# Optimization experiments

Measured on AMD Instinct MI355X. Metric: run time of the kernel, lower is better.

## Reference

```python
import jax, jax.numpy as jnp
import numpy as np

NAMES = ['tempo', 'chord', 'barbeat', 'type', 'pitch', 'duration', 'velocity']
VOCABS = [56, 135, 18, 4, 87, 18, 25]
EMBS = [128, 256, 64, 32, 512, 128, 128]
B, S, D, H, L, FF = 2, 2048, 512, 8, 8, 2048
HD = D // H
EPS = 1e-6


def _layernorm(x, g, b):
    m = x.mean(-1, keepdims=True)
    v = ((x - m) ** 2).mean(-1, keepdims=True)
    return (x - m) / jnp.sqrt(v + 1e-5) * g + b


def _rope(x, cos, sin):
    x1, x2 = jnp.split(x, 2, -1)
    return x * cos + jnp.concatenate([-x2, x1], -1) * sin


def _causal_linear_attn(q, k, v):
    # kernelized causal linear attention: phi = elu + 1, cumulative-sum normalization
    q = jax.nn.elu(q) + 1.0
    k = jax.nn.elu(k) + 1.0
    kv = jnp.cumsum(jnp.einsum('bshd,bshm->bshdm', k, v), axis=1)  # [B,S,H,HD,HD]
    z = 1.0 / (jnp.einsum('bshd,bshd->bsh', q, jnp.cumsum(k, axis=1)) + EPS)
    return jnp.einsum('bshd,bshdm->bshm', q, kv) * z[..., None]


def _forward(inputs, target, emb_tables, in_W, in_b, Wq, bq, Wk, bk, Wv, bv, Wo, bo,
             ln1_g, ln1_b, ln2_g, ln2_b, W1, b1, W2, b2, norm_g, norm_b, pWs, pbs, catW, catb):
    # multi-field embedding, each scaled by sqrt(d_emb) (CPEmbedding)
    embs = [emb_tables[i][inputs[..., i]] * jnp.sqrt(jnp.float32(EMBS[i])) for i in range(7)]
    x = jnp.concatenate(embs, -1) @ in_W + in_b  # [B,S,D]
    # PositionalEncoding: original indexes pe at position seq_len -> single d_model vector
    div = jnp.exp(jnp.arange(0, D, 2, dtype=jnp.float32) * (-np.log(10000.0) / D))
    pe = jnp.zeros((D,), jnp.float32).at[0::2].set(jnp.sin(S * div)).at[1::2].set(jnp.cos(S * div))
    x = x + pe
    # rotary tables for head_dim
    inv_freq = 1.0 / (10000.0 ** (jnp.arange(0, HD, 2, dtype=jnp.float32) / HD))
    fr = jnp.arange(S, dtype=jnp.float32)[:, None] * inv_freq[None, :]
    ang = jnp.concatenate([fr, fr], -1)  # [S,HD]
    cos = jnp.cos(ang)[None, :, None, :]
    sin = jnp.sin(ang)[None, :, None, :]
    for l in range(L):
        q = (x @ Wq[l] + bq[l]).reshape(B, S, H, HD)
        k = (x @ Wk[l] + bk[l]).reshape(B, S, H, HD)
        v = (x @ Wv[l] + bv[l]).reshape(B, S, H, HD)
        q = _rope(q, cos, sin)
        k = _rope(k, cos, sin)
        a = _causal_linear_attn(q, k, v).reshape(B, S, D) @ Wo[l] + bo[l]
        x = x + a
        y = x = _layernorm(x, ln1_g[l], ln1_b[l])
        y = jax.nn.gelu(y @ W1[l] + b1[l], approximate=False) @ W2[l] + b2[l]
        x = _layernorm(x + y, ln2_g[l], ln2_b[l])
    x = _layernorm(x, norm_g, norm_b)
    # MultiProj with teacher-forced type embedding (target branch)
    emb_t = emb_tables[3][target[..., 3]] * jnp.sqrt(jnp.float32(EMBS[3]))
    proj_type = (x @ pWs[3] + pbs[3]) * jnp.sqrt(jnp.float32(VOCABS[3]))  # from pre-concat x
    xc = jnp.concatenate([x, emb_t], -1) @ catW + catb
    outs = []
    for i in range(7):
        if i == 3:
            outs.append(proj_type)
        else:
            outs.append((xc @ pWs[i] + pbs[i]) * jnp.sqrt(jnp.float32(VOCABS[i])))
    return jnp.concatenate(outs, -1)  # [B,S,sum(VOCABS)=343]


def setup_inputs():
    key = jax.random.key(0)
    kit = iter(jax.random.split(key, 64))
    s = 0.02
    d = {}
    d['inputs'] = jax.random.randint(next(kit), (B, S, 7), 0, 4)
    d['target'] = jax.random.randint(next(kit), (B, S, 7), 0, 4)
    for i, n in enumerate(NAMES):
        d['emb_' + n] = jax.random.normal(next(kit), (VOCABS[i], EMBS[i]), jnp.float32) * s
    E = sum(EMBS)
    d['in_W'] = jax.random.normal(next(kit), (E, D)) * s
    d['in_b'] = jnp.zeros((D,))
    for nm, sh in [('Wq', (L, D, D)), ('Wk', (L, D, D)), ('Wv', (L, D, D)), ('Wo', (L, D, D)), ('W1', (L, D, FF)), ('W2', (L, FF, D))]:
        d[nm] = jax.random.normal(next(kit), sh) * s
    for nm, sh in [('bq', (L, D)), ('bk', (L, D)), ('bv', (L, D)), ('bo', (L, D)), ('b1', (L, FF)), ('b2', (L, D)), ('ln1_b', (L, D)), ('ln2_b', (L, D)), ('norm_b', (D,)), ('catb', (D,))]:
        d[nm] = jnp.zeros(sh)
    d['ln1_g'] = jnp.ones((L, D))
    d['ln2_g'] = jnp.ones((L, D))
    d['norm_g'] = jnp.ones((D,))
    for i, n in enumerate(NAMES):
        d['pW_' + n] = jax.random.normal(next(kit), (D, VOCABS[i])) * s
        d['pb_' + n] = jnp.zeros((VOCABS[i],))
    d['catW'] = jax.random.normal(next(kit), (D + 32, D)) * s
    return d


def reference(inputs, target, emb_tempo, emb_chord, emb_barbeat, emb_type, emb_pitch, emb_duration, emb_velocity,
              in_W, in_b, Wq, bq, Wk, bk, Wv, bv, Wo, bo, ln1_g, ln1_b, ln2_g, ln2_b, W1, b1, W2, b2,
              norm_g, norm_b, pW_tempo, pb_tempo, pW_chord, pb_chord, pW_barbeat, pb_barbeat, pW_type, pb_type,
              pW_pitch, pb_pitch, pW_duration, pb_duration, pW_velocity, pb_velocity, catW, catb):
    emb_tables = [emb_tempo, emb_chord, emb_barbeat, emb_type, emb_pitch, emb_duration, emb_velocity]
    pWs = [pW_tempo, pW_chord, pW_barbeat, pW_type, pW_pitch, pW_duration, pW_velocity]
    pbs = [pb_tempo, pb_chord, pb_barbeat, pb_type, pb_pitch, pb_duration, pb_velocity]
    return _forward(inputs, target, emb_tables, in_W, in_b, Wq, bq, Wk, bk, Wv, bv, Wo, bo,
                    ln1_g, ln1_b, ln2_g, ln2_b, W1, b1, W2, b2, norm_g, norm_b, pWs, pbs, catW, catb)
```

## Files before the change

kernel.cpp:

```cpp
#include <hip/hip_runtime.h>
#include <math.h>

typedef unsigned short u16;
typedef short bf16x8 __attribute__((ext_vector_type(8)));
typedef float f32x4 __attribute__((ext_vector_type(4)));
typedef u16 u16x4 __attribute__((ext_vector_type(4)));
typedef u16 u16x8 __attribute__((ext_vector_type(8)));

#define NB 2
#define NS 2048
#define ND 512
#define NH 8
#define NHD 64
#define NL 8
#define NFF 2048
#define NM (NB*NS)
#define NE 1248
#define NEP 1280
#define NXC 576
#define CHK 64
#define NCH (NS/CHK)
#define QKVW 1536

__device__ inline float b2f(u16 u){ union{ unsigned int i; float f;} x; x.i = ((unsigned int)u)<<16; return x.f; }
__device__ inline u16 f2b(float f){ union{ float f; unsigned int i;} x; x.f=f; unsigned int r = x.i + 0x7fffu + ((x.i>>16)&1u); return (u16)(r>>16); }

#define GLL(src, dst) __builtin_amdgcn_global_load_lds( \
    (__attribute__((address_space(1))) void*)(void*)(src), \
    (__attribute__((address_space(3))) void*)(dst), 16, 0, 0)

__global__ void k_embed(const int* __restrict__ inp,
    const float* __restrict__ e0, const float* __restrict__ e1, const float* __restrict__ e2,
    const float* __restrict__ e3, const float* __restrict__ e4, const float* __restrict__ e5,
    const float* __restrict__ e6, u16* __restrict__ xe)
{
  int row = blockIdx.x;
  int i0 = inp[row*7+0], i1 = inp[row*7+1], i2 = inp[row*7+2], i3 = inp[row*7+3],
      i4 = inp[row*7+4], i5 = inp[row*7+5], i6 = inp[row*7+6];
  size_t base = (size_t)row*NEP;
  for (int c = threadIdx.x; c < NEP; c += 256){
    float val = 0.f;
    if      (c < 128)  val = e0[i0*128 + c]        * 11.3137084990f;
    else if (c < 384)  val = e1[i1*256 + (c-128)]  * 16.0f;
    else if (c < 448)  val = e2[i2*64  + (c-384)]  * 8.0f;
    else if (c < 480)  val = e3[i3*32  + (c-448)]  * 5.6568542495f;
    else if (c < 992)  val = e4[i4*512 + (c-480)]  * 22.6274169980f;
    else if (c < 1120) val = e5[i5*128 + (c-992)]  * 11.3137084990f;
    else if (c < NE)   val = e6[i6*128 + (c-1120)] * 11.3137084990f;
    xe[base + c] = f2b(val);
  }
}

__device__ inline void trans_tile128(const float* __restrict__ W, u16* __restrict__ WT,
                                     int K, int N, int Kpad, int bx, int by){
  __shared__ u16 t[128*128];
  int tid = threadIdx.x;
  int k0 = by*128, n0 = bx*128;
  int c = tid & 31, sub = tid >> 5;
  #pragma unroll
  for (int p=0;p<16;p++){
    int kl = p*8 + sub;
    int k = k0 + kl;
    float4 v = {0.f,0.f,0.f,0.f};
    if (k < K) v = *(const float4*)(W + (size_t)k*N + n0 + c*4);
    #pragma unroll
    for (int i=0;i<4;i++){
      int n = c*4 + i;
      int g = (kl>>3) ^ (n & 15);
      t[n*128 + g*8 + (kl&7)] = f2b(((const float*)&v)[i]);
    }
  }
  __syncthreads();
  int kg = tid & 15, nsub = tid >> 4;
  #pragma unroll
  for (int p=0;p<8;p++){
    int nl = p*16 + nsub;
    int k = k0 + kg*8;
    if (k < Kpad)
      *(u16x8*)(WT + (size_t)(n0+nl)*Kpad + k) = *(const u16x8*)&t[nl*128 + ((kg ^ (nl&15))<<3)];
  }
}

__global__ void k_prepw(const float* __restrict__ Wq, const float* __restrict__ Wk,
                        const float* __restrict__ Wv, const float* __restrict__ Wo,
                        const float* __restrict__ in_W, const float* __restrict__ catW,
                        const float* __restrict__ W1, const float* __restrict__ W2,
                        u16* __restrict__ qkvoT, u16* __restrict__ inWT, u16* __restrict__ catWT,
                        u16* __restrict__ w1T, u16* __restrict__ w2T)
{
  int bid = blockIdx.x;
  if (bid < 512){
    int z = bid >> 4, r = bid & 15;
    int l = z >> 2, s2 = z & 3;
    const float* W = (s2==0?Wq:s2==1?Wk:s2==2?Wv:Wo) + (size_t)l*ND*ND;
    trans_tile128(W, qkvoT + (size_t)z*ND*ND, ND, ND, ND, r & 3, r >> 2);
  } else if (bid < 552){
    int r = bid - 512;
    trans_tile128(in_W, inWT, NE, ND, NEP, r & 3, r >> 2);
  } else if (bid < 572){
    int r = bid - 552;
    trans_tile128(catW, catWT, 544, ND, NXC, r & 3, r >> 2);
  } else if (bid < 1084){
    int r = bid - 572;
    int l = r >> 6; int rr = r & 63;
    trans_tile128(W1 + (size_t)l*ND*NFF, w1T + (size_t)l*ND*NFF, ND, NFF, ND, rr & 15, rr >> 4);
  } else {
    int r = bid - 1084;
    int l = r >> 6; int rr = r & 63;
    trans_tile128(W2 + (size_t)l*NFF*ND, w2T + (size_t)l*ND*NFF, NFF, ND, NFF, rr & 3, rr >> 2);
  }
}

__global__ void k_misc(float* __restrict__ rc, float* __restrict__ rs,
    const float* p0,const float* p1,const float* p2,const float* p3,
    const float* p4,const float* p5,const float* p6,
    const float* q0,const float* q1,const float* q2,const float* q3,
    const float* q4,const float* q5,const float* q6,
    u16* __restrict__ pwcT, float* __restrict__ pbc,
    u16* __restrict__ ptT, float* __restrict__ pbt,
    const float* __restrict__ bq, const float* __restrict__ bk, const float* __restrict__ bv,
    float* __restrict__ bqkv, const float* __restrict__ in_b, float* __restrict__ bias_in)
{
  int idx = blockIdx.x*256 + threadIdx.x;
  if (idx < NS*32){
    int s = idx >> 5, j = idx & 31;
    double inv = exp(-(double)(2*j) * log(10000.0) / (double)NHD);
    double ang = (double)s * inv;
    rc[idx] = (float)cos(ang);
    rs[idx] = (float)sin(ang);
  }
  const int off[8] = {0,56,191,209,213,300,318,343};
  {
    int col = idx >> 9, k = idx & 511;
    if (col < 384){
      u16 v = 0;
      if (col < 343){
        int f = 0;
        while (col >= off[f+1]) f++;
        int cc = col - off[f];
        int V = off[f+1]-off[f];
        const float* P = (f==0)?p0:(f==1)?p1:(f==2)?p2:(f==3)?p3:(f==4)?p4:(f==5)?p5:p6;
        v = f2b(P[(size_t)k*V + cc] * sqrtf((float)V));
      }
      pwcT[(size_t)col*512 + k] = v;
    }
    if (idx < 64*512){
      int n = idx >> 9;
      ptT[idx] = (n < 4) ? f2b(p3[(size_t)k*4 + n]*2.0f) : (u16)0;
    }
  }
  if (idx < 343){
    int c2 = idx, f = 0;
    while (c2 >= off[f+1]) f++;
    int cc = c2 - off[f]; int V = off[f+1]-off[f];
    const float* Q = (f==0)?q0:(f==1)?q1:(f==2)?q2:(f==3)?q3:(f==4)?q4:(f==5)?q5:q6;
    pbc[idx] = Q[cc]*sqrtf((float)V);
  }
  if (idx < 4) pbt[idx] = q3[idx]*2.0f;
  if (idx < NL*QKVW){
    int l = idx / QKVW, c = idx % QKVW;
    float v = (c < 512) ? bq[l*512 + c] : (c < 1024) ? bk[l*512 + c - 512] : bv[l*512 + c - 1024];
    bqkv[idx] = v;
  }
  if (idx < ND){
    double div = exp(-(double)(idx & ~1) * log(10000.0) / (double)ND);
    double ang = (double)NS * div;
    float pev = (idx & 1) ? (float)cos(ang) : (float)sin(ang);
    bias_in[idx] = in_b[idx] + pev;
  }
}

template<int ACT, int NT, int TM>
__global__ __launch_bounds__(256) void k_gemm(
    const u16* __restrict__ A, const u16* __restrict__ BT,
    const float* __restrict__ bias, float* __restrict__ Cf, u16* __restrict__ Cb,
    int N, int klen, int lda, int ldb, int ldc,
    int koff, float* __restrict__ Cf2,
    const float* __restrict__ rc, const float* __restrict__ rs)
{
  constexpr int MREP = TM/32;
  constexpr int BUFSZ = TM*64 + NT*32*64;
  __shared__ u16 SH[2*BUFSZ];
  int tid = threadIdx.x;
  int w = tid >> 6, lane = tid & 63;

  int kz = blockIdx.z;
  A  += (size_t)kz*koff;
  BT += (size_t)kz*koff;
  if (kz){ Cf = Cf2; bias = nullptr; }

  int nwg = gridDim.x*gridDim.y;
  int d = blockIdx.y*gridDim.x + blockIdx.x;
  int wl = ((nwg & 7) == 0) ? ((d & 7)*(nwg >> 3) + (d >> 3)) : d;
  int bx = wl % gridDim.x, by = wl / gridDim.x;
  int m0 = by*TM, n0 = bx*(NT*32);

  f32x4 acc[MREP][NT];
  #pragma unroll
  for (int m=0;m<MREP;m++)
    #pragma unroll
    for (int n=0;n<NT;n++) acc[m][n] = (f32x4){0.f,0.f,0.f,0.f};

  int lg = lane>>3;
  int cg = (lane&7) ^ lg;
  const u16* ag = A  + (size_t)(m0 + w*(TM/4) + lg)*lda + cg*8;
  const u16* bg = BT + (size_t)(n0 + w*(NT*8) + lg)*ldb + cg*8;
  int wr = (w>>1)*(TM/2), wc = (w&1)*(NT*16);
  int lr = lane & 15;
  int rx = lr & 7;
  int cb_ = lane >> 4;
  int g = lane >> 4;

  auto STAGE = [&](int buf, int k0){
    u16* As = SH + buf*BUFSZ;
    u16* Bs = As + TM*64;
    #pragma unroll
    for (int i=0;i<TM/32;i++)
      GLL(ag + (size_t)(i*8)*lda + k0, &As[(w*(TM/4) + i*8)*64]);
    #pragma unroll
    for (int j=0;j<NT;j++)
      GLL(bg + (size_t)(j*8)*ldb + k0, &Bs[(w*(NT*8) + j*8)*64]);
  };

  int nk = klen >> 6;
  STAGE(0, 0);
  __syncthreads();
  for (int t = 0; t < nk; ++t){
    int cur = t & 1;
    if (t+1 < nk) STAGE(cur^1, (t+1) << 6);
    const u16* As = SH + cur*BUFSZ;
    const u16* Bs = As + TM*64;
    #pragma unroll
    for (int kk=0;kk<2;kk++){
      int gA = ((kk*4 + cb_) ^ rx) * 8;
      bf16x8 af[MREP], bfr[NT];
      #pragma unroll
      for (int m=0;m<MREP;m++) af[m]  = *(const bf16x8*)&As[(wr + m*16 + lr)*64 + gA];
      #pragma unroll
      for (int n=0;n<NT;n++)   bfr[n] = *(const bf16x8*)&Bs[(wc + n*16 + lr)*64 + gA];
      #pragma unroll
      for (int m=0;m<MREP;m++)
        #pragma unroll
        for (int n=0;n<NT;n++)
          acc[m][n] = __builtin_amdgcn_mfma_f32_16x16x32_bf16(af[m], bfr[n], acc[m][n], 0,0,0);
    }
    __syncthreads();
  }

  if (ACT == 2){
    float* Cs = (float*)SH;
    #pragma unroll
    for (int n=0;n<NT;n++){
      int col = wc + n*16 + lr;
      float bv = bias ? bias[n0 + col] : 0.f;
      #pragma unroll
      for (int m=0;m<MREP;m++)
        #pragma unroll
        for (int r=0;r<4;r++)
          Cs[(wr + m*16 + g*4 + r)*64 + col] = acc[m][n][r] + bv;
    }
    __syncthreads();
    if (n0 < 1024){
      #pragma unroll
      for (int i=0;i<8;i++){
        int p = tid + i*256;
        int row = p >> 5, j = p & 31;
        float a1 = Cs[row*64 + j], a2 = Cs[row*64 + j + 32];
        int s = (m0 + row) & (NS-1);
        float c = rc[s*32+j], sn = rs[s*32+j];
        float r1 = a1*c - a2*sn, r2 = a2*c + a1*sn;
        Cb[(size_t)(m0+row)*ldc + n0 + j]      = f2b((r1 > 0.f) ? r1+1.f : expf(r1));
        Cb[(size_t)(m0+row)*ldc + n0 + j + 32] = f2b((r2 > 0.f) ? r2+1.f : expf(r2));
      }
    } else {
      #pragma unroll
      for (int i=0;i<16;i++){
        int p = tid + i*256;
        int row = p >> 6, c2 = p & 63;
        Cb[(size_t)(m0+row)*ldc + n0 + c2] = f2b(Cs[row*64 + c2]);
      }
    }
    return;
  }

  #pragma unroll
  for (int n=0;n<NT;n++){
    int col = n0 + wc + n*16 + lr;
    if (col < N){
      float bv = bias ? bias[col] : 0.f;
      #pragma unroll
      for (int m=0;m<MREP;m++){
        #pragma unroll
        for (int r=0;r<4;r++){
          int row = m0 + wr + m*16 + g*4 + r;
          float v = acc[m][n][r] + bv;
          if (ACT==1) v = 0.5f*v*(1.f+erff(v*0.70710678118654752f));
          if (Cf) Cf[(size_t)row*ldc + col] = v;
          if (Cb) Cb[(size_t)row*ldc + col] = f2b(v);
        }
      }
    }
  }
}

__global__ __launch_bounds__(256) void k_att1(const u16* __restrict__ qkv, float* __restrict__ pref){
  int c = blockIdx.x, h = blockIdx.y, b = blockIdx.z;
  __shared__ u16 Kt[64*64];
  __shared__ u16 Vt[80*64];
  int tid = threadIdx.x;
  {
    int t = tid & 63, dseg = (tid>>6)*16;
    const u16* kg = qkv + ((size_t)(b*NS + c*CHK + t))*QKVW + 512 + h*NHD + dseg;
    u16x8 k0 = *(const u16x8*)kg;
    u16x8 k1 = *(const u16x8*)(kg+8);
    u16x8 v0 = *(const u16x8*)(kg+512);
    u16x8 v1 = *(const u16x8*)(kg+520);
    #pragma unroll
    for (int e=0;e<8;e++){
      int d0 = dseg+e, d1 = dseg+8+e;
      Kt[(d0*64+t) ^ ((d0&7)<<3)] = k0[e];
      Kt[(d1*64+t) ^ ((d1&7)<<3)] = k1[e];
      Vt[(d0*64+t) ^ ((d0&7)<<3)] = v0[e];
      Vt[(d1*64+t) ^ ((d1&7)<<3)] = v1[e];
    }
    if (tid < 64) Vt[4096 + tid] = 0x3F80;
    for (int e = tid; e < 15*64; e += 256){
      int r = 65 + (e>>6), tt = e&63;
      Vt[(r*64+tt) ^ ((r&7)<<3)] = 0;
    }
  }
  __syncthreads();
  int lane = tid & 63, w = tid >> 6;
  int lr = lane & 15, lk = (lane>>4)*8;
  f32x4 acc[5];
  #pragma unroll
  for (int i=0;i<5;i++) acc[i] = (f32x4){0.f,0.f,0.f,0.f};
  #pragma unroll
  for (int kk=0;kk<2;kk++){
    int mcol = w*16 + lr;
    bf16x8 bfrag = *(const bf16x8*)&Kt[(mcol*64 + kk*32 + lk) ^ ((mcol&7)<<3)];
    #pragma unroll
    for (int fr=0; fr<5; fr++){
      int arow = fr*16 + lr;
      bf16x8 afrag = *(const bf16x8*)&Vt[(arow*64 + kk*32 + lk) ^ ((arow&7)<<3)];
      acc[fr] = __builtin_amdgcn_mfma_f32_16x16x32_bf16(afrag, bfrag, acc[fr], 0,0,0);
    }
  }
  size_t base = (((size_t)(b*NH + h))*NCH + c)*5120;
  int g = lane>>4;
  #pragma unroll
  for (int fr=0; fr<5; fr++)
    #pragma unroll
    for (int r=0;r<4;r++)
      pref[base + (fr*16 + g*4 + r)*64 + w*16 + lr] = acc[fr][r];
}

__global__ __launch_bounds__(256) void k_att2(const float* __restrict__ pref, u16* __restrict__ prefb){
  int bh = blockIdx.y;
  int e = blockIdx.x*256 + threadIdx.x;
  size_t base = (size_t)bh*NCH*5120 + e;
  int se = e ^ (((e>>6)&7)<<3);
  size_t sb = (size_t)bh*NCH*5120 + se;
  float v[NCH];
  #pragma unroll
  for (int c=0;c<NCH;c++) v[c] = pref[base + (size_t)c*5120];
  float run = 0.f;
  #pragma unroll
  for (int c=0;c<NCH;c++){ prefb[sb + (size_t)c*5120] = f2b(run); run += v[c]; }
}

__global__ __launch_bounds__(256) void k_att3(const u16* __restrict__ qkv,
    const u16* __restrict__ prefb, u16* __restrict__ outa)
{
  int c = blockIdx.x, h = blockIdx.y, b = blockIdx.z;
  __shared__ u16 Qs[4096], Ks[4096];
  __shared__ u16 Vt[5120], Ps[5120];
  __shared__ float dens[64];
  u16* Sm = Ks;
  int tid = threadIdx.x;
  int lane = tid & 63, w = tid >> 6;
  {
    int r8 = lane >> 3;
    int gsw = (lane & 7) ^ r8;
    const u16* qbase = qkv + ((size_t)(b*NS + c*CHK))*QKVW + h*NHD + gsw*8;
    #pragma unroll
    for (int half = 0; half < 2; half++){
      int rbase = w*16 + half*8;
      const u16* src = qbase + (size_t)(rbase + r8)*QKVW;
      GLL(src,       &Qs[rbase*64]);
      GLL(src + 512, &Ks[rbase*64]);
    }
    const u16* pb = prefb + (((size_t)(b*NH + h))*NCH + c)*5120 + lane*8;
    for (int ch = w; ch < 10; ch += 4)
      GLL(pb + ch*512, &Ps[ch*512]);
  }
  {
    int t = tid&63, dseg = (tid>>6)*16;
    const u16* vg = qkv + ((size_t)(b*NS + c*CHK + t))*QKVW + 1024 + h*NHD + dseg;
    u16x8 v0 = *(const u16x8*)vg;
    u16x8 v1 = *(const u16x8*)(vg+8);
    #pragma unroll
    for (int e=0;e<8;e++){
      int d0=dseg+e, d1=dseg+8+e;
      Vt[(d0*64+t)^((d0&7)<<3)] = v0[e];
      Vt[(d1*64+t)^((d1&7)<<3)] = v1[e];
    }
    if (tid<64) Vt[4096+tid] = 0x3F80;
    for (int e=tid; e<15*64; e+=256){
      int r = 65+(e>>6), tt = e&63;
      Vt[(r*64+tt)^((r&7)<<3)] = 0;
    }
  }
  __syncthreads();
  int lr = lane&15, lk = (lane>>4)*8, g = lane>>4;
  f32x4 sacc[4];
  #pragma unroll
  for (int i=0;i<4;i++) sacc[i] = (f32x4){0.f,0.f,0.f,0.f};
  int iq = w*16 + lr;
  #pragma unroll
  for (int kk=0;kk<2;kk++){
    bf16x8 bq = *(const bf16x8*)&Qs[(iq*64 + kk*32 + lk) ^ ((iq&7)<<3)];
    #pragma unroll
    for (int ft=0; ft<4; ft++){
      int tr = ft*16 + lr;
      bf16x8 ak = *(const bf16x8*)&Ks[(tr*64 + kk*32 + lk) ^ ((tr&7)<<3)];
      sacc[ft] = __builtin_amdgcn_mfma_f32_16x16x32_bf16(ak, bq, sacc[ft], 0,0,0);
    }
  }
  __syncthreads();
  #pragma unroll
  for (int ft=0; ft<4; ft++){
    int t0 = ft*16 + g*4;
    u16x4 pk;
    #pragma unroll
    for (int r=0;r<4;r++) pk[r] = f2b((t0+r <= iq) ? sacc[ft][r] : 0.f);
    *(u16x4*)&Sm[(iq*64 + t0) ^ ((iq&7)<<3)] = pk;
  }
  __syncthreads();
  f32x4 acc[5];
  #pragma unroll
  for (int i=0;i<5;i++) acc[i] = (f32x4){0.f,0.f,0.f,0.f};
  #pragma unroll
  for (int kk=0;kk<2;kk++){
    int sw = (iq&7)<<3;
    bf16x8 as = *(const bf16x8*)&Sm[(iq*64 + kk*32 + lk) ^ sw];
    bf16x8 aq = *(const bf16x8*)&Qs[(iq*64 + kk*32 + lk) ^ sw];
    #pragma unroll
    for (int c5=0;c5<5;c5++){
      int col = c5*16 + lr, sw2 = (col&7)<<3;
      bf16x8 bv = *(const bf16x8*)&Vt[(col*64 + kk*32 + lk) ^ sw2];
      bf16x8 bp = *(const bf16x8*)&Ps[(col*64 + kk*32 + lk) ^ sw2];
      acc[c5] = __builtin_amdgcn_mfma_f32_16x16x32_bf16(as, bv, acc[c5], 0,0,0);
      acc[c5] = __builtin_amdgcn_mfma_f32_16x16x32_bf16(aq, bp, acc[c5], 0,0,0);
    }
  }
  if (lr == 0){
    #pragma unroll
    for (int r=0;r<4;r++) dens[w*16 + g*4 + r] = acc[4][r];
  }
  __syncthreads();
  #pragma unroll
  for (int c5=0;c5<4;c5++){
    #pragma unroll
    for (int r=0;r<4;r++){
      int i = w*16 + g*4 + r;
      float z = 1.f/(dens[i] + 1e-6f);
      outa[((size_t)(b*NS + c*CHK + i))*ND + h*NHD + c5*16 + lr] = f2b(acc[c5][r]*z);
    }
  }
}

__global__ __launch_bounds__(256) void k_ln(const float* __restrict__ xin, const float* __restrict__ res,
    const float* __restrict__ res2, float* __restrict__ outx, u16* __restrict__ outb,
    const float* __restrict__ g, const float* __restrict__ bvec,
    const int* __restrict__ tgt, const float* __restrict__ embt, u16* __restrict__ xcb)
{
  int row = blockIdx.x, tid = threadIdx.x;
  size_t base = (size_t)row*ND;
  float v0 = xin[base+tid], v1 = xin[base+tid+256];
  if (res){ v0 += res[base+tid]; v1 += res[base+tid+256]; }
  if (res2){ v0 += res2[base+tid]; v1 += res2[base+tid+256]; }
  float s = v0+v1, ss2 = v0*v0 + v1*v1;
  #pragma unroll
  for (int o = 32; o >= 1; o >>= 1){
    s   += __shfl_down(s, o, 64);
    ss2 += __shfl_down(ss2, o, 64);
  }
  __shared__ float red[8];
  int wv = tid >> 6, ln = tid & 63;
  if (ln == 0){ red[wv] = s; red[4+wv] = ss2; }
  __syncthreads();
  float stot  = red[0]+red[1]+red[2]+red[3];
  float sstot = red[4]+red[5]+red[6]+red[7];
  float mean = stot * (1.0f/ND);
  float var  = sstot * (1.0f/ND) - mean*mean;
  float inv = 1.0f / sqrtf(var + 1e-5f);
  float o0 = (v0-mean)*inv*g[tid]     + bvec[tid];
  float o1 = (v1-mean)*inv*g[tid+256] + bvec[tid+256];
  outx[base+tid] = o0; outx[base+tid+256] = o1;
  if (outb){ outb[base+tid] = f2b(o0); outb[base+tid+256] = f2b(o1); }
  if (xcb){
    size_t xbse = (size_t)row*NXC;
    xcb[xbse+tid] = f2b(o0);
    xcb[xbse+tid+256] = f2b(o1);
    if (tid < 32){
      int id = tgt[row*7+3];
      xcb[xbse+512+tid] = f2b(embt[id*32+tid]*5.6568542495f);
      xcb[xbse+544+tid] = 0;
    }
  }
}

extern "C" void kernel_launch(void* const* d_in, const int* in_sizes, int n_in,
                              void* d_out, int out_size, void* d_ws, size_t ws_size,
                              hipStream_t stream)
{
  const int* inputs = (const int*)d_in[0];
  const int* target = (const int*)d_in[1];
  const float* emb[7];
  for (int i=0;i<7;i++) emb[i] = (const float*)d_in[2+i];
  const float* in_W  = (const float*)d_in[9];
  const float* in_b  = (const float*)d_in[10];
  const float* Wq = (const float*)d_in[11];
  const float* Wk = (const float*)d_in[12];
  const float* Wv = (const float*)d_in[13];
  const float* Wo = (const float*)d_in[14];
  const float* W1 = (const float*)d_in[15];
  const float* W2 = (const float*)d_in[16];
  const float* bq = (const float*)d_in[17];
  const float* bk = (const float*)d_in[18];
  const float* bv = (const float*)d_in[19];
  const float* bo = (const float*)d_in[20];
  const float* b1 = (const float*)d_in[21];
  const float* b2 = (const float*)d_in[22];
  const float* ln1_b = (const float*)d_in[23];
  const float* ln2_b = (const float*)d_in[24];
  const float* norm_b = (const float*)d_in[25];
  const float* catb   = (const float*)d_in[26];
  const float* ln1_g = (const float*)d_in[27];
  const float* ln2_g = (const float*)d_in[28];
  const float* norm_g = (const float*)d_in[29];
  const float* pW[7]; const float* pb[7];
  for (int i=0;i<7;i++){ pW[i]=(const float*)d_in[30+2*i]; pb[i]=(const float*)d_in[31+2*i]; }
  const float* catW = (const float*)d_in[44];
  float* outp = (float*)d_out;

  char* base = (char*)d_ws;
  size_t off = 0;
  auto alloc = [&](size_t bytes)->void*{ void* p = base + off; off += bytes; off = (off + 255) & ~(size_t)255; return p; };

  float* x    = (float*)alloc((size_t)NM*ND*4);
  u16*   xb   = (u16*)  alloc((size_t)NM*ND*2);
  u16*   qkvb = (u16*)  alloc((size_t)NM*QKVW*2);
  float* tb   = (float*)alloc((size_t)NM*ND*4);
  float* tb2  = (float*)alloc((size_t)NM*ND*4);
  u16*   ab   = (u16*)  alloc((size_t)NM*ND*2);
  u16*   hb   = (u16*)  alloc((size_t)NM*NFF*2);
  float* rc   = (float*)alloc((size_t)NS*32*4);
  float* rs   = (float*)alloc((size_t)NS*32*4);
  float* pref = (float*)alloc((size_t)NB*NH*NCH*5120*4);
  u16*  prefb = (u16*)  alloc((size_t)NB*NH*NCH*5120*2);
  u16*  qkvoT = (u16*)  alloc((size_t)NL*4*ND*ND*2);
  u16*  w1T   = (u16*)  alloc((size_t)NL*NFF*ND*2);
  u16*  w2T   = (u16*)  alloc((size_t)NL*ND*NFF*2);
  u16*  inWT  = (u16*)  alloc((size_t)ND*NEP*2);
  u16*  catWT = (u16*)  alloc((size_t)ND*NXC*2);
  u16*  pwcT  = (u16*)  alloc((size_t)384*512*2);
  float* pbc  = (float*)alloc(344*4);
  u16*  ptT   = (u16*)  alloc((size_t)64*512*2);
  float* pbt  = (float*)alloc(4*4);
  float* bqkv = (float*)alloc((size_t)NL*QKVW*4);
  float* bias_in = (float*)alloc(ND*4);
  u16*  xeb = hb;
  u16*  xcb = hb;
  u16*  ocb = hb + (size_t)NM*NXC;

  k_prepw<<<1596, 256, 0, stream>>>(Wq, Wk, Wv, Wo, in_W, catW, W1, W2,
                                    qkvoT, inWT, catWT, w1T, w2T);
  k_misc<<<768, 256, 0, stream>>>(rc, rs,
      pW[0],pW[1],pW[2],pW[3],pW[4],pW[5],pW[6],
      pb[0],pb[1],pb[2],pb[3],pb[4],pb[5],pb[6],
      pwcT, pbc, ptT, pbt, bq, bk, bv, bqkv, in_b, bias_in);

  k_embed<<<NM, 256, 0, stream>>>(inputs, emb[0],emb[1],emb[2],emb[3],emb[4],emb[5],emb[6], xeb);
  k_gemm<0,2,64><<<dim3(8,64,1), 256, 0, stream>>>(xeb, inWT, bias_in, x, xb,
      ND, NEP, NEP, NEP, ND, 0, nullptr, nullptr, nullptr);

  dim3 agrid(NCH, NH, NB);
  for (int l = 0; l < NL; l++){
    const u16* woT = qkvoT + (size_t)(l*4+3)*ND*ND;
    k_gemm<2,2,64><<<dim3(24,64,1), 256, 0, stream>>>(xb, qkvoT + (size_t)l*4*ND*ND,
        bqkv + l*QKVW, nullptr, qkvb, QKVW, ND, ND, ND, QKVW, 0, nullptr, rc, rs);
    k_att1<<<agrid, 256, 0, stream>>>(qkvb, pref);
    k_att2<<<dim3(20,16), 256, 0, stream>>>(pref, prefb);
    k_att3<<<agrid, 256, 0, stream>>>(qkvb, prefb, ab);
    k_gemm<0,2,64><<<dim3(8,64,2), 256, 0, stream>>>(ab, woT, bo + l*ND, tb, nullptr,
        ND, 256, ND, ND, ND, 256, tb2, nullptr, nullptr);
    k_ln<<<NM, 256, 0, stream>>>(x, tb, tb2, x, xb, ln1_g + l*ND, ln1_b + l*ND,
                                 nullptr, nullptr, nullptr);
    k_gemm<1,2,64><<<dim3(32,64,1), 256, 0, stream>>>(xb, w1T + (size_t)l*NFF*ND,
        b1 + l*NFF, nullptr, hb, NFF, ND, ND, ND, NFF, 0, nullptr, nullptr, nullptr);
    k_gemm<0,2,64><<<dim3(8,64,2), 256, 0, stream>>>(hb, w2T + (size_t)l*ND*NFF,
        b2 + l*ND, tb, nullptr, ND, 1024, NFF, NFF, ND, 1024, tb2, nullptr, nullptr);
    k_ln<<<NM, 256, 0, stream>>>(x, tb, tb2, x, xb, ln2_g + l*ND, ln2_b + l*ND,
                                 nullptr, nullptr, nullptr);
  }

  k_ln<<<NM, 256, 0, stream>>>(x, nullptr, nullptr, x, xb, norm_g, norm_b,
                               target, emb[3], xcb);

  k_gemm<0,2,64><<<dim3(8,64,1), 256, 0, stream>>>(xcb, catWT, catb, nullptr, ocb,
      ND, NXC, NXC, NXC, ND, 0, nullptr, nullptr, nullptr);
  k_gemm<0,2,64><<<dim3(6,64,1), 256, 0, stream>>>(ocb, pwcT, pbc, outp, nullptr,
      343, ND, ND, ND, 343, 0, nullptr, nullptr, nullptr);
  k_gemm<0,2,64><<<dim3(1,64,1), 256, 0, stream>>>(xb, ptT, pbt, outp + 209, nullptr,
      4, ND, ND, ND, 343, 0, nullptr, nullptr, nullptr);
}
```

Before: 833.2 us.

## Drop GEMM LDS double buffering and vectorize weight transpose LDS writes

The GEMM kernel goes from a double-buffered LDS pipeline (prefetching the next K tile while computing the current one) to a single buffer that is loaded, synchronized, then consumed each iteration. This halves shared memory per block and may allow higher occupancy, but load latency is no longer hidden behind MFMA work within a block. The weight transpose tile now gathers 8 consecutive k values per column in registers and writes them to LDS as one 16-byte vector instead of scalar stores.

```diff
diff --git a/kernel.cpp b/kernel.cpp
--- a/kernel.cpp
+++ b/kernel.cpp
@@ -58,26 +58,32 @@
   int k0 = by*128, n0 = bx*128;
   int c = tid & 31, sub = tid >> 5;
   #pragma unroll
-  for (int p=0;p<16;p++){
-    int kl = p*8 + sub;
-    int k = k0 + kl;
-    float4 v = {0.f,0.f,0.f,0.f};
-    if (k < K) v = *(const float4*)(W + (size_t)k*N + n0 + c*4);
+  for (int half=0; half<2; half++){
+    int kg = sub + half*8;
+    u16 r0[8], r1[8], r2[8], r3[8];
+    #pragma unroll
+    for (int j=0;j<8;j++){
+      int k = k0 + kg*8 + j;
+      float4 v = {0.f,0.f,0.f,0.f};
+      if (k < K) v = *(const float4*)(W + (size_t)k*N + n0 + c*4);
+      r0[j] = f2b(v.x); r1[j] = f2b(v.y); r2[j] = f2b(v.z); r3[j] = f2b(v.w);
+    }
     #pragma unroll
     for (int i=0;i<4;i++){
       int n = c*4 + i;
-      int g = (kl>>3) ^ (n & 15);
-      t[n*128 + g*8 + (kl&7)] = f2b(((const float*)&v)[i]);
+      int g = kg ^ (n & 15);
+      const u16* rp = (i==0)?r0:(i==1)?r1:(i==2)?r2:r3;
+      *(u16x8*)&t[n*128 + g*8] = *(const u16x8*)rp;
     }
   }
   __syncthreads();
-  int kg = tid & 15, nsub = tid >> 4;
+  int kg2 = tid & 15, nsub = tid >> 4;
   #pragma unroll
   for (int p=0;p<8;p++){
     int nl = p*16 + nsub;
-    int k = k0 + kg*8;
+    int k = k0 + kg2*8;
     if (k < Kpad)
-      *(u16x8*)(WT + (size_t)(n0+nl)*Kpad + k) = *(const u16x8*)&t[nl*128 + ((kg ^ (nl&15))<<3)];
+      *(u16x8*)(WT + (size_t)(n0+nl)*Kpad + k) = *(const u16x8*)&t[nl*128 + ((kg2 ^ (nl&15))<<3)];
   }
 }
 
@@ -179,8 +185,9 @@
     const float* __restrict__ rc, const float* __restrict__ rs)
 {
   constexpr int MREP = TM/32;
-  constexpr int BUFSZ = TM*64 + NT*32*64;
-  __shared__ u16 SH[2*BUFSZ];
+  __shared__ u16 SH[TM*64 + NT*32*64];
+  u16* As = SH;
+  u16* Bs = SH + TM*64;
   int tid = threadIdx.x;
   int w = tid >> 6, lane = tid & 63;
 
@@ -211,25 +218,16 @@
   int cb_ = lane >> 4;
   int g = lane >> 4;
 
-  auto STAGE = [&](int buf, int k0){
-    u16* As = SH + buf*BUFSZ;
-    u16* Bs = As + TM*64;
+  int nk = klen >> 6;
+  for (int t = 0; t < nk; ++t){
+    int k0 = t << 6;
     #pragma unroll
     for (int i=0;i<TM/32;i++)
       GLL(ag + (size_t)(i*8)*lda + k0, &As[(w*(TM/4) + i*8)*64]);
     #pragma unroll
     for (int j=0;j<NT;j++)
       GLL(bg + (size_t)(j*8)*ldb + k0, &Bs[(w*(NT*8) + j*8)*64]);
-  };
-
-  int nk = klen >> 6;
-  STAGE(0, 0);
-  __syncthreads();
-  for (int t = 0; t < nk; ++t){
-    int cur = t & 1;
-    if (t+1 < nk) STAGE(cur^1, (t+1) << 6);
-    const u16* As = SH + cur*BUFSZ;
-    const u16* Bs = As + TM*64;
+    __syncthreads();
     #pragma unroll
     for (int kk=0;kk<2;kk++){
       int gA = ((kk*4 + cb_) ^ rx) * 8;
```

Measured after the change: 828.7 us. Within noise of the previous version (-0.5%).
